# Performance work log

Hardware: AMD Instinct MI355X
Metric: run time of the kernel (lower is better)

The kernel has to match this reference:

```python
import jax, jax.numpy as jnp
import numpy as np

K = 5  # top_kernel_size

def circular_pad(x, p):
    # x: [B, C, H, W] -> [B, C, H+2p, W+2p], torch 'circular' == numpy 'wrap'
    return jnp.pad(x, ((0, 0), (0, 0), (p, p), (p, p)), mode='wrap')

def unfold(x, k):
    # x: [B, C, Hp, Wp] (already padded). Returns [B, H*W, C*k*k] with
    # torch.nn.functional.unfold ordering (c slowest, then kh, kw).
    B, C, Hp, Wp = x.shape
    H, W = Hp - k + 1, Wp - k + 1
    patches = jnp.stack([x[:, :, i:i + H, j:j + W]
                         for i in range(k) for j in range(k)], axis=2)  # [B,C,k*k,H,W]
    return patches.reshape(B, C * k * k, H * W).transpose(0, 2, 1)

def build_table(recording, walls, k):
    # recording: [T, C, H, W], walls: [H, W] -> [T*H*W, (C+1)*k*k]
    T, C, H, W = recording.shape
    walls_rep = jnp.broadcast_to(walls[None, None], (T, 1, H, W))
    rec = jnp.concatenate([recording, walls_rep], axis=1)  # [T, C+1, H, W]
    unf = unfold(circular_pad(rec, k // 2), k)              # [T, H*W, D]
    return unf.reshape(T * H * W, -1)

def nn_step(cur, src_table, tgt_table, k):
    # cur: [B, C, H, W]; brute-force L2 NN over src_table rows, gather center
    # pixel of the matched *next-frame* patch from tgt_table.
    B, C, H, W = cur.shape
    xu = unfold(circular_pad(cur, k // 2), k)  # [B, HW, D]
    # squared L2 distance (argmin-equivalent to torch.cdist p=2)
    d2 = (jnp.sum(xu * xu, axis=-1, keepdims=True)
          + jnp.sum(src_table * src_table, axis=-1)[None, None, :]
          - 2.0 * jnp.einsum('bnd,md->bnm', xu, src_table))  # [B, HW, N]
    idx = jnp.argmin(d2, axis=2)          # [B, HW]
    val = tgt_table[idx]                   # [B, HW, D]
    mid = (k * k) // 2
    val = val.reshape(B, H * W, C, k * k)[:, :, :, mid]  # center pixel -> [B,HW,C]
    return val.transpose(0, 2, 1).reshape(B, C, H, W)

def setup_inputs() -> dict:
    key = jax.random.key(0)
    k1, k2, k3 = jax.random.split(key, 3)
    return {
        'x': jax.random.normal(k1, (1, 3, 3, 48, 48), dtype=jnp.float32),
        'recording': jax.random.normal(k2, (16, 3, 48, 48), dtype=jnp.float32),
        'walls': jax.random.uniform(k3, (48, 48), dtype=jnp.float32),
    }

def reference(x, recording, walls):
    B, T, C, H, W = x.shape
    table = build_table(recording, walls, K)   # [T_rec*HW, D]
    HW = H * W
    src = table[:-HW]   # source patches (all frames but last)
    tgt = table[HW:]    # next-frame patches (shift by one frame)
    walls_rep = jnp.broadcast_to(walls[None, None, None], (B, T, 1, H, W))
    x = jnp.concatenate([x, walls_rep], axis=2)  # [B, T, C+1, H, W]

    def step(carry, target):
        val = nn_step(carry, src, tgt, K)
        loss = jnp.mean((val - target) ** 2)
        return val, (val, loss)

    targets = jnp.moveaxis(x[:, 1:], 1, 0)  # [T-1, B, C+1, H, W]
    _, (vals, losses) = jax.lax.scan(step, x[:, 0], targets)
    all_steps = jnp.concatenate([x[:, :1], jnp.moveaxis(vals, 0, 1)], axis=1)
    return all_steps[:, :, :-1], jnp.mean(losses)  # drop wall channel
```

## Files before the change

### kernel.cpp

```cpp
#include <hip/hip_runtime.h>

#define HW 2304
#define W48 48
#define NT 15
#define RST 17
#define RS_SIZE (W48 * RST)
#define RXW 128

__global__ __launch_bounds__(256) void prep_kernel(
    const float* __restrict__ x, const float* __restrict__ rec,
    const float* __restrict__ walls,
    float4* __restrict__ rec4, float4* __restrict__ rec4x,
    float4* __restrict__ cur0, float* __restrict__ dout,
    unsigned long long* __restrict__ best_part)
{
    int id = blockIdx.x * 256 + threadIdx.x;
    if (id < 16 * HW) {
        int t = id / HW, p = id % HW;
        int y = p / W48, xx = p % W48;
        float4 v = make_float4(rec[(t * 3 + 0) * HW + p],
                               rec[(t * 3 + 1) * HW + p],
                               rec[(t * 3 + 2) * HW + p],
                               walls[p]);
        rec4[id] = v;
        float4* rowd = rec4x + (size_t)(t * W48 + y) * RXW;
        rowd[xx] = v;
        rowd[xx + 48] = v;
        if (xx < 32) rowd[xx + 96] = v;
    }
    if (id < HW) {
        cur0[id] = make_float4(x[0 * HW + id], x[1 * HW + id], x[2 * HW + id],
                               walls[id]);
    }
    if (id < 3 * HW) {
        dout[id] = x[id];
    }
    if (id < NT * HW) {
        best_part[id] = ~0ULL;
    }
}

template <int CTL>
__device__ __forceinline__ float dppf(float v)
{
    return __int_as_float(__builtin_amdgcn_update_dpp(
        0, __float_as_int(v), CTL, 0xF, 0xF, false));
}
#define ROR1  0x121
#define ROR15 0x12F

__global__ __launch_bounds__(256) void dist_kernel(
    const float4* __restrict__ rec4x, const float4* __restrict__ cur4,
    unsigned long long* __restrict__ best_part)
{
    __shared__ float Rs[4 * RS_SIZE];

    const int tid = threadIdx.x;
    const int b   = blockIdx.x;
    const int t   = b / 384;
    const int rem = b % 384;
    const int sy  = rem >> 3;
    const int q   = rem & 7;
    const int yq  = q >> 1;
    const int sx0 = (q & 1) * 24;

    const int rid = tid >> 4;
    const int cA  = tid & 15;
    const int x0  = 3 * cA;
    int qy = yq * 12 + rid - 2;
    if (qy < 0) qy += W48;
    if (qy >= W48) qy -= W48;
    int ry = qy + sy; if (ry >= W48) ry -= W48;

    const float4* curRow = cur4 + qy * W48;
    const float4 c0 = curRow[x0 + 0];
    const float4 c1 = curRow[x0 + 1];
    const float4 c2 = curRow[x0 + 2];
    const float2 cw0a = make_float2(c0.x, c0.y), cw0b = make_float2(c0.z, c0.w);
    const float2 cw1a = make_float2(c1.x, c1.y), cw1b = make_float2(c1.z, c1.w);
    const float2 cw2a = make_float2(c2.x, c2.y), cw2b = make_float2(c2.z, c2.w);

    const int cb = x0 + sx0;
    const float4* rb = rec4x + (size_t)(t * W48 + ry) * RXW + cb;

    float2 q0a, q0b, q1a, q1b, q2a, q2b, q3a, q3b, q4a, q4b, q5a, q5b;
    {
        float4 v;
        v = rb[0]; q0a = make_float2(v.x, v.y); q0b = make_float2(v.z, v.w);
        v = rb[1]; q1a = make_float2(v.x, v.y); q1b = make_float2(v.z, v.w);
        v = rb[2]; q2a = make_float2(v.x, v.y); q2b = make_float2(v.z, v.w);
        v = rb[3]; q3a = make_float2(v.x, v.y); q3b = make_float2(v.z, v.w);
        v = rb[4]; q4a = make_float2(v.x, v.y); q4b = make_float2(v.z, v.w);
        v = rb[5]; q5a = make_float2(v.x, v.y); q5b = make_float2(v.z, v.w);
    }

    const bool cact = tid < 192;
    const int xc  = tid % W48;
    const int y0C = 3 * (tid / W48);
    const int qyB = yq * 12 + y0C;
    unsigned int mb0 = 0, mb1 = 0, mb2 = 0;
    if (cact) {
        int o0 = qyB + 0 + sy; if (o0 >= W48) o0 -= W48;
        int o1 = qyB + 1 + sy; if (o1 >= W48) o1 -= W48;
        int o2 = qyB + 2 + sy; if (o2 >= W48) o2 -= W48;
        mb0 = (unsigned)(t * HW + o0 * W48);
        mb1 = (unsigned)(t * HW + o1 * W48);
        mb2 = (unsigned)(t * HW + o2 * W48);
    }
    int rx = xc + sx0; if (rx >= W48) rx -= W48;

    unsigned long long bst0 = ~0ULL, bst1 = ~0ULL, bst2 = ~0ULL;

#define DIFFP(F, CAa, CAb, WAa, WAb) do {                                   \
        float2 dA_ = (CAa) - (WAa);                                         \
        float2 dB_ = (CAb) - (WAb);                                         \
        float2 s_  = dA_ * dA_ + dB_ * dB_;                                 \
        F = s_.x + s_.y;                                                    \
    } while (0)

#define COLMIN(BUF, RX) do {                                                \
        const float* rp = &Rs[(BUF) * RS_SIZE + xc * RST + y0C];            \
        float rv0 = rp[0], rv1 = rp[1], rv2 = rp[2], rv3 = rp[3];           \
        float rv4 = rp[4], rv5 = rp[5], rv6 = rp[6];                        \
        float U_ = rv2 + rv3 + rv4;                                         \
        float D0 = rv0 + rv1 + U_;                                          \
        float D1 = rv1 + U_ + rv5;                                          \
        float D2 = U_ + rv5 + rv6;                                          \
        unsigned long long pk;                                              \
        pk = ((unsigned long long)__float_as_uint(D0) << 32) |              \
             (mb0 + (unsigned)(RX));                                        \
        bst0 = pk < bst0 ? pk : bst0;                                       \
        pk = ((unsigned long long)__float_as_uint(D1) << 32) |              \
             (mb1 + (unsigned)(RX));                                        \
        bst1 = pk < bst1 ? pk : bst1;                                       \
        pk = ((unsigned long long)__float_as_uint(D2) << 32) |              \
             (mb2 + (unsigned)(RX));                                        \
        bst2 = pk < bst2 ? pk : bst2;                                       \
    } while (0)

#define STEP2(PB, J, A0a, A0b, A1a, A1b, A2a, A2b, A3a, A3b) do {           \
        float F0a, F1a, F2a, F0b, F1b, F2b;                                 \
        DIFFP(F0a, cw0a, cw0b, A0a, A0b);                                   \
        DIFFP(F1a, cw1a, cw1b, A1a, A1b);                                   \
        DIFFP(F2a, cw2a, cw2b, A2a, A2b);                                   \
        DIFFP(F0b, cw0a, cw0b, A1a, A1b);                                   \
        DIFFP(F1b, cw1a, cw1b, A2a, A2b);                                   \
        DIFFP(F2b, cw2a, cw2b, A3a, A3b);                                   \
        float Fm2a = dppf<ROR1>(F1a);                                       \
        float Fm1a = dppf<ROR1>(F2a);                                       \
        float F3a  = dppf<ROR15>(F0a);                                      \
        float F4a  = dppf<ROR15>(F1a);                                      \
        float Fm2b = dppf<ROR1>(F1b);                                       \
        float Fm1b = dppf<ROR1>(F2b);                                       \
        float F3b  = dppf<ROR15>(F0b);                                      \
        float F4b  = dppf<ROR15>(F1b);                                      \
        float Ta  = F0a + F1a + F2a;                                        \
        float R0a = Fm2a + Fm1a + Ta;                                       \
        float R1a = Fm1a + Ta + F3a;                                        \
        float R2a = Ta + F3a + F4a;                                         \
        float Tb  = F0b + F1b + F2b;                                        \
        float R0b = Fm2b + Fm1b + Tb;                                       \
        float R1b = Fm1b + Tb + F3b;                                        \
        float R2b = Tb + F3b + F4b;                                         \
        {                                                                   \
            float* wa = &Rs[(PB) * RS_SIZE + x0 * RST + rid];               \
            wa[0 * RST] = R0a; wa[1 * RST] = R1a; wa[2 * RST] = R2a;        \
            float* wb = &Rs[((PB) + 1) * RS_SIZE + x0 * RST + rid];         \
            wb[0 * RST] = R0b; wb[1 * RST] = R1b; wb[2 * RST] = R2b;        \
        }                                                                   \
        {                                                                   \
            float4 v_;                                                      \
            v_ = rb[J];                                                     \
            A0a = make_float2(v_.x, v_.y); A0b = make_float2(v_.z, v_.w);   \
            v_ = rb[(J) + 1];                                               \
            A1a = make_float2(v_.x, v_.y); A1b = make_float2(v_.z, v_.w);   \
        }                                                                   \
        __syncthreads();                                                    \
        if (cact) {                                                         \
            int rxB = rx + 1; if (rxB >= W48) rxB -= W48;                   \
            COLMIN(PB, rx);                                                 \
            COLMIN((PB) + 1, rxB);                                          \
            rx = rxB + 1; if (rx >= W48) rx -= W48;                         \
        } else {                                                            \
            rx += 2; if (rx >= W48) rx -= W48;                              \
        }                                                                   \
    } while (0)

    STEP2(0,  6, q0a, q0b, q1a, q1b, q2a, q2b, q3a, q3b);
    STEP2(2,  8, q2a, q2b, q3a, q3b, q4a, q4b, q5a, q5b);
    STEP2(0, 10, q4a, q4b, q5a, q5b, q0a, q0b, q1a, q1b);
    STEP2(2, 12, q0a, q0b, q1a, q1b, q2a, q2b, q3a, q3b);
    STEP2(0, 14, q2a, q2b, q3a, q3b, q4a, q4b, q5a, q5b);
    STEP2(2, 16, q4a, q4b, q5a, q5b, q0a, q0b, q1a, q1b);
    STEP2(0, 18, q0a, q0b, q1a, q1b, q2a, q2b, q3a, q3b);
    STEP2(2, 20, q2a, q2b, q3a, q3b, q4a, q4b, q5a, q5b);
    STEP2(0, 22, q4a, q4b, q5a, q5b, q0a, q0b, q1a, q1b);
    STEP2(2, 24, q0a, q0b, q1a, q1b, q2a, q2b, q3a, q3b);
    STEP2(0, 26, q2a, q2b, q3a, q3b, q4a, q4b, q5a, q5b);
    STEP2(2, 28, q4a, q4b, q5a, q5b, q0a, q0b, q1a, q1b);
#undef STEP2
#undef COLMIN
#undef DIFFP

    if (cact) {
        unsigned long long* bt = best_part + (size_t)t * HW + qyB * W48 + xc;
        atomicMin(&bt[0 * W48], bst0);
        atomicMin(&bt[1 * W48], bst1);
        atomicMin(&bt[2 * W48], bst2);
    }
}

__global__ __launch_bounds__(256) void gather_kernel(
    unsigned long long* __restrict__ best_part,
    const float4* __restrict__ rec4, const float* __restrict__ x,
    const float* __restrict__ walls,
    float4* __restrict__ curnext, float* __restrict__ dout,
    float* __restrict__ err, int step)
{
    int p = blockIdx.x * 256 + threadIdx.x;
    if (p >= HW) return;
    unsigned long long bestv = ~0ULL;
#pragma unroll
    for (int j = 0; j < NT; j++) {
        unsigned long long v = best_part[(size_t)j * HW + p];
        bestv = v < bestv ? v : bestv;
    }
#pragma unroll
    for (int j = 0; j < NT; j++) {
        best_part[(size_t)j * HW + p] = ~0ULL;
    }
    unsigned int m = (unsigned int)bestv;
    int t = m / HW, qq = m % HW;
    float4 v = rec4[(t + 1) * HW + qq];
    curnext[p] = v;
    dout[(step + 1) * 3 * HW + 0 * HW + p] = v.x;
    dout[(step + 1) * 3 * HW + 1 * HW + p] = v.y;
    dout[(step + 1) * 3 * HW + 2 * HW + p] = v.z;
    float t0 = x[((step + 1) * 3 + 0) * HW + p];
    float t1 = x[((step + 1) * 3 + 1) * HW + p];
    float t2 = x[((step + 1) * 3 + 2) * HW + p];
    float t3 = walls[p];
    float e = (v.x - t0) * (v.x - t0) + (v.y - t1) * (v.y - t1) +
              (v.z - t2) * (v.z - t2) + (v.w - t3) * (v.w - t3);
    err[step * HW + p] = e;
}

__global__ __launch_bounds__(256) void loss_kernel(
    const float* __restrict__ err, float* __restrict__ dout)
{
    __shared__ float ssum[256];
    float s = 0.f;
    for (int i = threadIdx.x; i < 2 * HW; i += 256) s += err[i];
    ssum[threadIdx.x] = s;
    __syncthreads();
    for (int w = 128; w > 0; w >>= 1) {
        if (threadIdx.x < w) ssum[threadIdx.x] += ssum[threadIdx.x + w];
        __syncthreads();
    }
    if (threadIdx.x == 0) dout[9 * HW] = ssum[0] / 18432.0f;
}

extern "C" void kernel_launch(void* const* d_in, const int* in_sizes, int n_in,
                              void* d_out, int out_size, void* d_ws,
                              size_t ws_size, hipStream_t stream)
{
    const float* x     = (const float*)d_in[0];
    const float* rec   = (const float*)d_in[1];
    const float* walls = (const float*)d_in[2];
    float* dout = (float*)d_out;

    char* ws = (char*)d_ws;
    float4* rec4  = (float4*)ws;
    float4* rec4x = (float4*)(ws + 589824);
    float4* curb  = (float4*)(ws + 589824 + 1572864);
    float*  err   = (float*)(ws + 589824 + 1572864 + 110592);
    unsigned long long* best_part =
        (unsigned long long*)(ws + 589824 + 1572864 + 110592 + 18432);

    prep_kernel<<<144, 256, 0, stream>>>(x, rec, walls, rec4, rec4x, curb,
                                         dout, best_part);
    for (int step = 0; step < 2; step++) {
        dist_kernel<<<NT * W48 * 8, 256, 0, stream>>>(rec4x, curb + step * HW,
                                                      best_part);
        gather_kernel<<<9, 256, 0, stream>>>(best_part, rec4, x, walls,
                                             curb + (step + 1) * HW, dout, err,
                                             step);
    }
    loss_kernel<<<1, 256, 0, stream>>>(err, dout);
}
```

Measured before the change: 132.3 us.

## Use persistent dist_kernel with atomic work queue and fp64 fmin packed argmin

Replaces the one-block-per-item grid of 5760 blocks with a persistent grid of 2048 blocks. Each block pulls work items from a global atomic counter, and the counter is zeroed in prep_kernel, one per step. The packed distance/index argmin now uses double-precision fmin on reinterpreted bits instead of a 64-bit integer compare/select. The aim is to cut block launch and tail overhead and to shorten the min reduction. The costs are an extra atomic plus __syncthreads per item, and fmin over bit patterns that must behave like unsigned ordering, which holds only for non-negative finite values.

```diff
diff --git a/kernel.cpp b/kernel.cpp
--- a/kernel.cpp
+++ b/kernel.cpp
@@ -6,13 +6,15 @@
 #define RST 17
 #define RS_SIZE (W48 * RST)
 #define RXW 128
+#define NITEMS 5760
 
 __global__ __launch_bounds__(256) void prep_kernel(
     const float* __restrict__ x, const float* __restrict__ rec,
     const float* __restrict__ walls,
     float4* __restrict__ rec4, float4* __restrict__ rec4x,
     float4* __restrict__ cur0, float* __restrict__ dout,
-    unsigned long long* __restrict__ best_part)
+    unsigned long long* __restrict__ best_part,
+    unsigned int* __restrict__ ctr)
 {
     int id = blockIdx.x * 256 + threadIdx.x;
     if (id < 16 * HW) {
@@ -38,6 +40,9 @@
     if (id < NT * HW) {
         best_part[id] = ~0ULL;
     }
+    if (id < 2) {
+        ctr[id] = 0u;
+    }
 }
 
 template <int CTL>
@@ -51,65 +56,21 @@
 
 __global__ __launch_bounds__(256) void dist_kernel(
     const float4* __restrict__ rec4x, const float4* __restrict__ cur4,
-    unsigned long long* __restrict__ best_part)
+    unsigned long long* __restrict__ best_part,
+    unsigned int* __restrict__ ctr)
 {
     __shared__ float Rs[4 * RS_SIZE];
+    __shared__ unsigned int sItem;
 
     const int tid = threadIdx.x;
-    const int b   = blockIdx.x;
-    const int t   = b / 384;
-    const int rem = b % 384;
-    const int sy  = rem >> 3;
-    const int q   = rem & 7;
-    const int yq  = q >> 1;
-    const int sx0 = (q & 1) * 24;
 
     const int rid = tid >> 4;
     const int cA  = tid & 15;
     const int x0  = 3 * cA;
-    int qy = yq * 12 + rid - 2;
-    if (qy < 0) qy += W48;
-    if (qy >= W48) qy -= W48;
-    int ry = qy + sy; if (ry >= W48) ry -= W48;
-
-    const float4* curRow = cur4 + qy * W48;
-    const float4 c0 = curRow[x0 + 0];
-    const float4 c1 = curRow[x0 + 1];
-    const float4 c2 = curRow[x0 + 2];
-    const float2 cw0a = make_float2(c0.x, c0.y), cw0b = make_float2(c0.z, c0.w);
-    const float2 cw1a = make_float2(c1.x, c1.y), cw1b = make_float2(c1.z, c1.w);
-    const float2 cw2a = make_float2(c2.x, c2.y), cw2b = make_float2(c2.z, c2.w);
-
-    const int cb = x0 + sx0;
-    const float4* rb = rec4x + (size_t)(t * W48 + ry) * RXW + cb;
-
-    float2 q0a, q0b, q1a, q1b, q2a, q2b, q3a, q3b, q4a, q4b, q5a, q5b;
-    {
-        float4 v;
-        v = rb[0]; q0a = make_float2(v.x, v.y); q0b = make_float2(v.z, v.w);
-        v = rb[1]; q1a = make_float2(v.x, v.y); q1b = make_float2(v.z, v.w);
-        v = rb[2]; q2a = make_float2(v.x, v.y); q2b = make_float2(v.z, v.w);
-        v = rb[3]; q3a = make_float2(v.x, v.y); q3b = make_float2(v.z, v.w);
-        v = rb[4]; q4a = make_float2(v.x, v.y); q4b = make_float2(v.z, v.w);
-        v = rb[5]; q5a = make_float2(v.x, v.y); q5b = make_float2(v.z, v.w);
-    }
-
     const bool cact = tid < 192;
     const int xc  = tid % W48;
     const int y0C = 3 * (tid / W48);
-    const int qyB = yq * 12 + y0C;
-    unsigned int mb0 = 0, mb1 = 0, mb2 = 0;
-    if (cact) {
-        int o0 = qyB + 0 + sy; if (o0 >= W48) o0 -= W48;
-        int o1 = qyB + 1 + sy; if (o1 >= W48) o1 -= W48;
-        int o2 = qyB + 2 + sy; if (o2 >= W48) o2 -= W48;
-        mb0 = (unsigned)(t * HW + o0 * W48);
-        mb1 = (unsigned)(t * HW + o1 * W48);
-        mb2 = (unsigned)(t * HW + o2 * W48);
-    }
-    int rx = xc + sx0; if (rx >= W48) rx -= W48;
-
-    unsigned long long bst0 = ~0ULL, bst1 = ~0ULL, bst2 = ~0ULL;
+    const double DMAXD = __longlong_as_double(0x7FEFFFFFFFFFFFFFLL);
 
 #define DIFFP(F, CAa, CAb, WAa, WAb) do {                                   \
         float2 dA_ = (CAa) - (WAa);                                         \
@@ -126,16 +87,15 @@
         float D0 = rv0 + rv1 + U_;                                          \
         float D1 = rv1 + U_ + rv5;                                          \
         float D2 = U_ + rv5 + rv6;                                          \
-        unsigned long long pk;                                              \
-        pk = ((unsigned long long)__float_as_uint(D0) << 32) |              \
-             (mb0 + (unsigned)(RX));                                        \
-        bst0 = pk < bst0 ? pk : bst0;                                       \
-        pk = ((unsigned long long)__float_as_uint(D1) << 32) |              \
-             (mb1 + (unsigned)(RX));                                        \
-        bst1 = pk < bst1 ? pk : bst1;                                       \
-        pk = ((unsigned long long)__float_as_uint(D2) << 32) |              \
-             (mb2 + (unsigned)(RX));                                        \
-        bst2 = pk < bst2 ? pk : bst2;                                       \
+        bst0 = fmin(bst0, __longlong_as_double(                             \
+            ((unsigned long long)__float_as_uint(D0) << 32) |               \
+            (mb0 + (unsigned)(RX))));                                       \
+        bst1 = fmin(bst1, __longlong_as_double(                             \
+            ((unsigned long long)__float_as_uint(D1) << 32) |               \
+            (mb1 + (unsigned)(RX))));                                       \
+        bst2 = fmin(bst2, __longlong_as_double(                             \
+            ((unsigned long long)__float_as_uint(D2) << 32) |               \
+            (mb2 + (unsigned)(RX))));                                       \
     } while (0)
 
 #define STEP2(PB, J, A0a, A0b, A1a, A1b, A2a, A2b, A3a, A3b) do {           \
@@ -186,28 +146,90 @@
         }                                                                   \
     } while (0)
 
-    STEP2(0,  6, q0a, q0b, q1a, q1b, q2a, q2b, q3a, q3b);
-    STEP2(2,  8, q2a, q2b, q3a, q3b, q4a, q4b, q5a, q5b);
-    STEP2(0, 10, q4a, q4b, q5a, q5b, q0a, q0b, q1a, q1b);
-    STEP2(2, 12, q0a, q0b, q1a, q1b, q2a, q2b, q3a, q3b);
-    STEP2(0, 14, q2a, q2b, q3a, q3b, q4a, q4b, q5a, q5b);
-    STEP2(2, 16, q4a, q4b, q5a, q5b, q0a, q0b, q1a, q1b);
-    STEP2(0, 18, q0a, q0b, q1a, q1b, q2a, q2b, q3a, q3b);
-    STEP2(2, 20, q2a, q2b, q3a, q3b, q4a, q4b, q5a, q5b);
-    STEP2(0, 22, q4a, q4b, q5a, q5b, q0a, q0b, q1a, q1b);
-    STEP2(2, 24, q0a, q0b, q1a, q1b, q2a, q2b, q3a, q3b);
-    STEP2(0, 26, q2a, q2b, q3a, q3b, q4a, q4b, q5a, q5b);
-    STEP2(2, 28, q4a, q4b, q5a, q5b, q0a, q0b, q1a, q1b);
+    for (;;) {
+        if (tid == 0) sItem = atomicAdd(ctr, 1u);
+        __syncthreads();
+        const unsigned int item = sItem;
+        if (item >= NITEMS) break;
+
+        const int t   = item / 384;
+        const int rem = item % 384;
+        const int sy  = rem >> 3;
+        const int q   = rem & 7;
+        const int yq  = q >> 1;
+        const int sx0 = (q & 1) * 24;
+
+        int qy = yq * 12 + rid - 2;
+        if (qy < 0) qy += W48;
+        if (qy >= W48) qy -= W48;
+        int ry = qy + sy; if (ry >= W48) ry -= W48;
+
+        const float4* curRow = cur4 + qy * W48;
+        const float4 c0 = curRow[x0 + 0];
+        const float4 c1 = curRow[x0 + 1];
+        const float4 c2 = curRow[x0 + 2];
+        const float2 cw0a = make_float2(c0.x, c0.y);
+        const float2 cw0b = make_float2(c0.z, c0.w);
+        const float2 cw1a = make_float2(c1.x, c1.y);
+        const float2 cw1b = make_float2(c1.z, c1.w);
+        const float2 cw2a = make_float2(c2.x, c2.y);
+        const float2 cw2b = make_float2(c2.z, c2.w);
+
+        const int cb = x0 + sx0;
+        const float4* rb = rec4x + (size_t)(t * W48 + ry) * RXW + cb;
+
+        float2 q0a, q0b, q1a, q1b, q2a, q2b, q3a, q3b, q4a, q4b, q5a, q5b;
+        {
+            float4 v;
+            v = rb[0]; q0a = make_float2(v.x, v.y); q0b = make_float2(v.z, v.w);
+            v = rb[1]; q1a = make_float2(v.x, v.y); q1b = make_float2(v.z, v.w);
+            v = rb[2]; q2a = make_float2(v.x, v.y); q2b = make_float2(v.z, v.w);
+            v = rb[3]; q3a = make_float2(v.x, v.y); q3b = make_float2(v.z, v.w);
+            v = rb[4]; q4a = make_float2(v.x, v.y); q4b = make_float2(v.z, v.w);
+            v = rb[5]; q5a = make_float2(v.x, v.y); q5b = make_float2(v.z, v.w);
+        }
+
+        const int qyB = yq * 12 + y0C;
+        unsigned int mb0 = 0, mb1 = 0, mb2 = 0;
+        if (cact) {
+            int o0 = qyB + 0 + sy; if (o0 >= W48) o0 -= W48;
+            int o1 = qyB + 1 + sy; if (o1 >= W48) o1 -= W48;
+            int o2 = qyB + 2 + sy; if (o2 >= W48) o2 -= W48;
+            mb0 = (unsigned)(t * HW + o0 * W48);
+            mb1 = (unsigned)(t * HW + o1 * W48);
+            mb2 = (unsigned)(t * HW + o2 * W48);
+        }
+        int rx = xc + sx0; if (rx >= W48) rx -= W48;
+
+        double bst0 = DMAXD, bst1 = DMAXD, bst2 = DMAXD;
+
+        STEP2(0,  6, q0a, q0b, q1a, q1b, q2a, q2b, q3a, q3b);
+        STEP2(2,  8, q2a, q2b, q3a, q3b, q4a, q4b, q5a, q5b);
+        STEP2(0, 10, q4a, q4b, q5a, q5b, q0a, q0b, q1a, q1b);
+        STEP2(2, 12, q0a, q0b, q1a, q1b, q2a, q2b, q3a, q3b);
+        STEP2(0, 14, q2a, q2b, q3a, q3b, q4a, q4b, q5a, q5b);
+        STEP2(2, 16, q4a, q4b, q5a, q5b, q0a, q0b, q1a, q1b);
+        STEP2(0, 18, q0a, q0b, q1a, q1b, q2a, q2b, q3a, q3b);
+        STEP2(2, 20, q2a, q2b, q3a, q3b, q4a, q4b, q5a, q5b);
+        STEP2(0, 22, q4a, q4b, q5a, q5b, q0a, q0b, q1a, q1b);
+        STEP2(2, 24, q0a, q0b, q1a, q1b, q2a, q2b, q3a, q3b);
+        STEP2(0, 26, q2a, q2b, q3a, q3b, q4a, q4b, q5a, q5b);
+        STEP2(2, 28, q4a, q4b, q5a, q5b, q0a, q0b, q1a, q1b);
+
+        if (cact) {
+            unsigned long long* bt =
+                best_part + (size_t)t * HW + qyB * W48 + xc;
+            atomicMin(&bt[0 * W48], (unsigned long long)
+                      __double_as_longlong(bst0));
+            atomicMin(&bt[1 * W48], (unsigned long long)
+                      __double_as_longlong(bst1));
+            atomicMin(&bt[2 * W48], (unsigned long long)
+                      __double_as_longlong(bst2));
+        }
+    }
 #undef STEP2
 #undef COLMIN
 #undef DIFFP
-
-    if (cact) {
-        unsigned long long* bt = best_part + (size_t)t * HW + qyB * W48 + xc;
-        atomicMin(&bt[0 * W48], bst0);
-        atomicMin(&bt[1 * W48], bst1);
-        atomicMin(&bt[2 * W48], bst2);
-    }
 }
 
 __global__ __launch_bounds__(256) void gather_kernel(
@@ -276,12 +298,14 @@
     float*  err   = (float*)(ws + 589824 + 1572864 + 110592);
     unsigned long long* best_part =
         (unsigned long long*)(ws + 589824 + 1572864 + 110592 + 18432);
+    unsigned int* ctr =
+        (unsigned int*)(ws + 589824 + 1572864 + 110592 + 18432 + 276480);
 
     prep_kernel<<<144, 256, 0, stream>>>(x, rec, walls, rec4, rec4x, curb,
-                                         dout, best_part);
+                                         dout, best_part, ctr);
     for (int step = 0; step < 2; step++) {
-        dist_kernel<<<NT * W48 * 8, 256, 0, stream>>>(rec4x, curb + step * HW,
-                                                      best_part);
+        dist_kernel<<<2048, 256, 0, stream>>>(rec4x, curb + step * HW,
+                                              best_part, ctr + step);
         gather_kernel<<<9, 256, 0, stream>>>(best_part, rec4, x, walls,
                                              curb + (step + 1) * HW, dout, err,
                                              step);
```

Result: slower. 218.3 us (+65.0%).
